# Optimization experiments

Measured on AMD Instinct MI355X. Metric: run time of the kernel, lower is better.

## Reference

```python
import jax, jax.numpy as jnp
import numpy as np

B, N, C = 4, 4096, 512
H = 8          # num_heads
M = 64         # num_landmarks
HD = C // H    # head_dim = 64
N_ITER = 6     # Newton-Schulz iterations (Nystromformer default)


def iterative_inv(mat):
    # mat: [B, H, M, M]; Nystromformer pseudo-inverse via Newton-Schulz.
    I = jnp.eye(mat.shape[-1], dtype=mat.dtype)
    K = mat
    # global-max initialization (original Nystromformer 'original' init)
    V = K.swapaxes(-1, -2) / (jnp.max(jnp.sum(K, axis=-2)) * jnp.max(jnp.sum(K, axis=-1)))
    for _ in range(N_ITER):
        KV = jnp.matmul(K, V)
        V = 0.25 * jnp.matmul(V, 13.0 * I - jnp.matmul(KV, 15.0 * I - jnp.matmul(KV, 7.0 * I - KV)))
    return V


def setup_inputs() -> dict:
    key = jax.random.key(0)
    k1, k2, k3, k4 = jax.random.split(key, 4)
    s = C ** -0.5
    return {
        "x": jax.random.normal(k1, (B, N, C), dtype=jnp.float32),
        "qkv_w": jax.random.normal(k2, (3 * C, C), dtype=jnp.float32) * s,
        "proj_w": jax.random.normal(k3, (C, C), dtype=jnp.float32) * s,
        "proj_b": jax.random.normal(k4, (C,), dtype=jnp.float32) * 0.01,
        "epoch": 1,
    }


def reference(x, qkv_w, proj_w, proj_b, epoch):
    b, n, c = x.shape
    hd = c // H
    qkv = (x @ qkv_w.T).reshape(b, n, 3, H, hd).transpose(2, 0, 3, 1, 4)  # [3,B,H,N,hd]
    Q, K, V = qkv[0], qkv[1], qkv[2]
    scale = 1.0 / np.sqrt(np.sqrt(hd)).astype(np.float32)
    Q = Q * scale
    K = K * scale
    # landmark pooling: mean over segments of length N // M
    Ql = Q.reshape(b, H, M, n // M, hd).mean(axis=-2)  # [B,H,M,hd]
    Kl = K.reshape(b, H, M, n // M, hd).mean(axis=-2)
    kernel_1 = jax.nn.softmax(jnp.einsum('bhnd,bhmd->bhnm', Q, Kl), axis=-1)   # [B,H,N,M]
    kernel_2 = jax.nn.softmax(jnp.einsum('bhmd,bhld->bhml', Ql, Kl), axis=-1)  # [B,H,M,M]
    kernel_3 = jax.nn.softmax(jnp.einsum('bhmd,bhnd->bhmn', Ql, K), axis=-1)   # [B,H,M,N]
    X = jnp.matmul(jnp.matmul(kernel_1, iterative_inv(kernel_2)), jnp.matmul(kernel_3, V))
    X = X.transpose(0, 2, 1, 3).reshape(b, n, c)
    return X @ proj_w.T + proj_b
```

## Files before the change

kernel.cpp:

```cpp
#include <hip/hip_runtime.h>
#include <hip/hip_bf16.h>
#include <stdint.h>

#define QSZe 8388608ull

typedef __attribute__((ext_vector_type(8))) short bf16x8;
typedef __attribute__((ext_vector_type(4))) float f32x4;
typedef const __attribute__((address_space(1))) unsigned int* gas1_t;
typedef __attribute__((address_space(3))) unsigned int* las3_t;

__device__ __forceinline__ float bf2f(unsigned short u) {
  return __uint_as_float(((unsigned int)u) << 16);
}
__device__ __forceinline__ unsigned short f2bf(float f) {
  unsigned int u = __float_as_uint(f);
  unsigned int r = (u + 0x7FFFu + ((u >> 16) & 1u)) >> 16;
  return (unsigned short)r;
}
__device__ __forceinline__ void gload_lds16(const void* g, void* l) {
  __builtin_amdgcn_global_load_lds((gas1_t)g, (las3_t)l, 16, 0, 0);
}

__global__ void detect_bias(const unsigned short* __restrict__ raw_x,
                            const void* __restrict__ raw_b,
                            float* __restrict__ cbf,
                            unsigned int* __restrict__ flag) {
  __shared__ unsigned int fl;
  int t = threadIdx.x;
  if (t < 64) {
    int big = 0;
    for (int i = t; i < 256; i += 64) {
      int e = (raw_x[i] >> 7) & 0xFF;
      if (e >= 0x8F) big = 1;
    }
    unsigned long long b = __ballot(big);
    if (t == 0) {
      fl = (b != 0ull) ? 1u : 0u;
      flag[0] = fl;
    }
  }
  __syncthreads();
  unsigned int f = fl;
  for (int i = t; i < 512; i += 256)
    cbf[i] = f ? ((const float*)raw_b)[i]
               : bf2f(((const unsigned short*)raw_b)[i]);
}

__global__ __launch_bounds__(256) void conv_all(
    const void* __restrict__ rx, const void* __restrict__ rwq,
    const void* __restrict__ rwp, unsigned short* __restrict__ cx,
    unsigned short* __restrict__ cwq, unsigned short* __restrict__ cwp,
    const unsigned int* __restrict__ flag) {
  int gid = blockIdx.x * 256 + threadIdx.x;
  const void* src;
  unsigned short* dst;
  int i8;
  if (gid < 1048576) {
    src = rx; dst = cx; i8 = gid * 8;
  } else if (gid < 1146880) {
    src = rwq; dst = cwq; i8 = (gid - 1048576) * 8;
  } else {
    src = rwp; dst = cwp; i8 = (gid - 1146880) * 8;
  }
  if (flag[0]) {
    const float* f = (const float*)src;
    float4 a = *(const float4*)(f + i8);
    float4 b = *(const float4*)(f + i8 + 4);
    unsigned short o[8] = {f2bf(a.x), f2bf(a.y), f2bf(a.z), f2bf(a.w),
                           f2bf(b.x), f2bf(b.y), f2bf(b.z), f2bf(b.w)};
    *(uint4*)(dst + i8) = *(const uint4*)o;
  } else {
    *(uint4*)(dst + i8) = *(const uint4*)((const unsigned short*)src + i8);
  }
}

__device__ __forceinline__ void mmB(const unsigned short* A_R,
                                    const unsigned short* B_T,
                                    unsigned short* out_R,
                                    unsigned short* out_T, int wave, int lane,
                                    float s, float dg, float a7,
                                    const unsigned short* Aelt) {
  const int fr = lane & 15, fq = lane >> 4;
  bf16x8 af0 = *(const bf16x8*)&A_R[(wave * 16 + fr) * 64 + fq * 8];
  bf16x8 af1 = *(const bf16x8*)&A_R[(wave * 16 + fr) * 64 + 32 + fq * 8];
  f32x4 acc[4] = {};
#pragma unroll
  for (int j = 0; j < 4; j++) {
    bf16x8 b0 = *(const bf16x8*)&B_T[(j * 16 + fr) * 64 + fq * 8];
    bf16x8 b1 = *(const bf16x8*)&B_T[(j * 16 + fr) * 64 + 32 + fq * 8];
    acc[j] = __builtin_amdgcn_mfma_f32_16x16x32_bf16(af0, b0, acc[j], 0, 0, 0);
    acc[j] = __builtin_amdgcn_mfma_f32_16x16x32_bf16(af1, b1, acc[j], 0, 0, 0);
  }
  float ael[4][4];
  if (Aelt) {
#pragma unroll
    for (int j = 0; j < 4; j++)
#pragma unroll
      for (int r = 0; r < 4; r++)
        ael[j][r] = bf2f(Aelt[(wave * 16 + fq * 4 + r) * 64 + j * 16 + fr]);
  }
  __syncthreads();
#pragma unroll
  for (int j = 0; j < 4; j++) {
    int col = j * 16 + fr;
    unsigned short pack[4];
#pragma unroll
    for (int r = 0; r < 4; r++) {
      int row = wave * 16 + fq * 4 + r;
      float v = s * acc[j][r] + ((row == col) ? dg : 0.0f);
      if (Aelt) v += a7 * ael[j][r];
      unsigned short bv = f2bf(v);
      if (out_R) out_R[row * 64 + col] = bv;
      pack[r] = bv;
    }
    if (out_T)
      *(uint2*)&out_T[col * 64 + wave * 16 + fq * 4] = *(const uint2*)pack;
  }
}

__global__ __launch_bounds__(256) void qkv_gemm_mfma(
    const unsigned short* __restrict__ w, const unsigned short* __restrict__ x,
    unsigned short* __restrict__ qkv, float* __restrict__ Ql,
    float* __restrict__ Kl, unsigned short* __restrict__ Qlb,
    unsigned short* __restrict__ Klb) {
  __shared__ __align__(16) unsigned short At[128 * 64];
  __shared__ __align__(16) unsigned short Bt[128 * 64];
  const int t = threadIdx.x;
  const int lane = t & 63, wave = t >> 6;
  const int wf = wave >> 1, wt = wave & 1;
  const int f0 = blockIdx.x * 128, n0g = blockIdx.y * 128;
  const int srow = lane >> 3, skc = ((lane & 7) ^ srow) * 8;
  const int fr = lane & 15, fq = lane >> 4;
  const int rsw = fr & 7;
  f32x4 acc[4][4] = {};

  for (int k0 = 0; k0 < 512; k0 += 64) {
#pragma unroll
    for (int s = 0; s < 4; s++) {
      int inst = wave * 4 + s;
      int row = inst * 8 + srow;
      gload_lds16(w + (size_t)(f0 + row) * 512 + k0 + skc, &At[inst * 512]);
      gload_lds16(x + (size_t)(n0g + row) * 512 + k0 + skc, &Bt[inst * 512]);
    }
    __syncthreads();
#pragma unroll
    for (int kk = 0; kk < 64; kk += 32) {
      bf16x8 af[4], bxf[4];
#pragma unroll
      for (int i = 0; i < 4; i++)
        af[i] = *(const bf16x8*)&At[(wf * 64 + i * 16 + fr) * 64 +
                                    ((((kk >> 3) + fq) ^ rsw) << 3)];
#pragma unroll
      for (int j = 0; j < 4; j++)
        bxf[j] = *(const bf16x8*)&Bt[(wt * 64 + j * 16 + fr) * 64 +
                                     ((((kk >> 3) + fq) ^ rsw) << 3)];
#pragma unroll
      for (int i = 0; i < 4; i++)
#pragma unroll
        for (int j = 0; j < 4; j++)
          acc[i][j] = __builtin_amdgcn_mfma_f32_16x16x32_bf16(
              af[i], bxf[j], acc[i][j], 0, 0, 0);
    }
    __syncthreads();
  }
  const int fbase = f0 + wf * 64;
  const int which = fbase >> 9;
  const int h = (fbase >> 6) & 7;
  const float scale = (which < 2) ? 0.3535533905932738f : 1.0f;
  const int b_ = n0g >> 12;
  const int bh = b_ * 8 + h;
  const int m_loc = ((n0g + wt * 64) & 4095) >> 6;
#pragma unroll
  for (int i = 0; i < 4; i++) {
    int d0 = i * 16 + fq * 4;
#pragma unroll
    for (int j = 0; j < 4; j++) {
      int nn = (n0g + wt * 64 + j * 16 + fr) & 4095;
      unsigned short pack[4];
#pragma unroll
      for (int r = 0; r < 4; r++) pack[r] = f2bf(acc[i][j][r] * scale);
      *(uint2*)&qkv[(size_t)which * QSZe + ((size_t)bh * 4096 + nn) * 64 +
                    d0] = *(const uint2*)pack;
    }
  }
  if (which < 2) {
    const float ps = scale * (1.0f / 64.0f);
#pragma unroll
    for (int i = 0; i < 4; i++) {
      float sm[4];
#pragma unroll
      for (int r = 0; r < 4; r++)
        sm[r] = acc[i][0][r] + acc[i][1][r] + acc[i][2][r] + acc[i][3][r];
#pragma unroll
      for (int mask = 1; mask < 16; mask <<= 1)
#pragma unroll
        for (int r = 0; r < 4; r++) sm[r] += __shfl_xor(sm[r], mask, 64);
      if (fr == 0) {
        int d0 = i * 16 + fq * 4;
        float4 v4 = make_float4(sm[0] * ps, sm[1] * ps, sm[2] * ps, sm[3] * ps);
        unsigned short pk[4] = {f2bf(v4.x), f2bf(v4.y), f2bf(v4.z), f2bf(v4.w)};
        size_t off = (size_t)bh * 4096 + m_loc * 64 + d0;
        if (which == 0) {
          *(float4*)&Ql[off] = v4;
          *(uint2*)&Qlb[off] = *(const uint2*)pk;
        } else {
          *(float4*)&Kl[off] = v4;
          *(uint2*)&Klb[off] = *(const uint2*)pk;
        }
      }
    }
  }
}

__global__ __launch_bounds__(256) void k2_kernel(
    const float* __restrict__ Ql, const float* __restrict__ Kl,
    float* __restrict__ k2, unsigned int* __restrict__ gstat) {
  __shared__ float KlT[64 * 64];
  __shared__ float Ps[64][65];
  int t = threadIdx.x;
  int lane = t & 63, wv = t >> 6;
  int bh = blockIdx.x;
#pragma unroll
  for (int i = 0; i < 16; i++) {
    int idx = i * 256 + t;
    KlT[(idx & 63) * 64 + (idx >> 6)] = Kl[bh * 4096 + idx];
  }
  __syncthreads();
  for (int r = wv * 16; r < wv * 16 + 16; r++) {
    float qv = Ql[(bh * 64 + r) * 64 + lane];
    float acc = 0.f;
#pragma unroll
    for (int k = 0; k < 64; k++) acc += __shfl(qv, k, 64) * KlT[k * 64 + lane];
    float mx = acc;
#pragma unroll
    for (int o = 32; o > 0; o >>= 1) mx = fmaxf(mx, __shfl_xor(mx, o, 64));
    float e = __expf(acc - mx);
    float s = e;
#pragma unroll
    for (int o = 32; o > 0; o >>= 1) s += __shfl_xor(s, o, 64);
    float p = e / s;
    k2[(bh * 64 + r) * 64 + lane] = p;
    Ps[r][lane] = p;
  }
  __syncthreads();
  float val = 0.f;
  if (t < 64) {
    for (int r = 0; r < 64; r++) val += Ps[r][t];
  } else if (t < 128) {
    int r = t - 64;
    for (int c = 0; c < 64; c++) val += Ps[r][c];
  }
  float mv = val;
#pragma unroll
  for (int o = 32; o > 0; o >>= 1) mv = fmaxf(mv, __shfl_xor(mv, o, 64));
  if (t == 0) atomicMax(gstat + 0, __float_as_uint(mv));
  if (t == 64) atomicMax(gstat + 1, __float_as_uint(mv));
}

__global__ __launch_bounds__(256) void k3_mfma(
    const unsigned short* __restrict__ Qlb,
    const unsigned short* __restrict__ qkv, float* __restrict__ Wp,
    float* __restrict__ sp) {
  __shared__ __align__(16) unsigned short Et[64 * 136];
  __shared__ __align__(16) unsigned short Vt[64 * 136];
  __shared__ float scol_l[4][64];
  const int t = threadIdx.x;
  const int lane = t & 63, wave = t >> 6;
  const int fr = lane & 15, fq = lane >> 4;
  const int slab = blockIdx.x, bh = blockIdx.y;
  const int n_base = slab * 512;
  const unsigned short* Kb = qkv + QSZe + (size_t)bh * 262144;
  const unsigned short* Vb = qkv + 2 * QSZe + (size_t)bh * 262144;
  const unsigned short* Qlp = Qlb + bh * 4096;

  bf16x8 qb[2][4];
#pragma unroll
  for (int h = 0; h < 2; h++)
#pragma unroll
    for (int j = 0; j < 4; j++)
      qb[h][j] = *(const bf16x8*)(Qlp + (j * 16 + fr) * 64 + h * 32 + fq * 8);

  f32x4 accW[4] = {};
  float scol[4] = {0.f, 0.f, 0.f, 0.f};

  for (int sc = 0; sc < 4; sc++) {
    const int n0 = n_base + sc * 128;
    {
      int n = t & 127, dg = t >> 7;
#pragma unroll
      for (int i = 0; i < 4; i++) {
        int d0 = (dg + 2 * i) * 8;
        uint4 v = *(const uint4*)(Vb + (size_t)(n0 + n) * 64 + d0);
        const unsigned short* s = (const unsigned short*)&v;
#pragma unroll
        for (int u = 0; u < 8; u++) Vt[(d0 + u) * 136 + n] = s[u];
      }
    }
    f32x4 acc[2][4] = {};
#pragma unroll
    for (int i = 0; i < 2; i++) {
      const unsigned short* Kr =
          Kb + (size_t)(n0 + wave * 32 + i * 16 + fr) * 64;
      bf16x8 a0 = *(const bf16x8*)(Kr + fq * 8);
      bf16x8 a1 = *(const bf16x8*)(Kr + 32 + fq * 8);
#pragma unroll
      for (int j = 0; j < 4; j++) {
        acc[i][j] = __builtin_amdgcn_mfma_f32_16x16x32_bf16(a0, qb[0][j],
                                                            acc[i][j], 0, 0, 0);
        acc[i][j] = __builtin_amdgcn_mfma_f32_16x16x32_bf16(a1, qb[1][j],
                                                            acc[i][j], 0, 0, 0);
      }
    }
#pragma unroll
    for (int i = 0; i < 2; i++)
#pragma unroll
      for (int j = 0; j < 4; j++) {
        unsigned short pack[4];
        float s4 = 0.f;
#pragma unroll
        for (int r = 0; r < 4; r++) {
          float e = __expf(acc[i][j][r]);
          s4 += e;
          pack[r] = f2bf(e);
        }
        scol[j] += s4;
        *(uint2*)&Et[(j * 16 + fr) * 136 + wave * 32 + i * 16 + fq * 4] =
            *(const uint2*)pack;
      }
    __syncthreads();
#pragma unroll
    for (int kk = 0; kk < 128; kk += 32) {
      bf16x8 ap = *(const bf16x8*)&Et[(wave * 16 + fr) * 136 + kk + fq * 8];
#pragma unroll
      for (int j = 0; j < 4; j++) {
        bf16x8 bv = *(const bf16x8*)&Vt[(j * 16 + fr) * 136 + kk + fq * 8];
        accW[j] =
            __builtin_amdgcn_mfma_f32_16x16x32_bf16(ap, bv, accW[j], 0, 0, 0);
      }
    }
    __syncthreads();
  }
#pragma unroll
  for (int j = 0; j < 4; j++) {
    float s = scol[j];
    s += __shfl_xor(s, 16, 64);
    s += __shfl_xor(s, 32, 64);
    if (fq == 0) scol_l[wave][j * 16 + fr] = s;
  }
  __syncthreads();
  if (t < 64)
    sp[(bh * 8 + slab) * 64 + t] =
        scol_l[0][t] + scol_l[1][t] + scol_l[2][t] + scol_l[3][t];
  float* wpo = Wp + ((size_t)bh * 8 + slab) * 4096;
#pragma unroll
  for (int j = 0; j < 4; j++)
#pragma unroll
    for (int r = 0; r < 4; r++)
      wpo[(wave * 16 + fq * 4 + r) * 64 + j * 16 + fr] = accW[j][r];
}

__global__ __launch_bounds__(256) void ns_kernel(
    const float* __restrict__ k2g, const unsigned int* __restrict__ gstat,
    const float* __restrict__ Wp, const float* __restrict__ sp,
    unsigned short* __restrict__ Ztb) {
  __shared__ __align__(16) unsigned short L[8 * 4096];
  __shared__ float ssum[64];
  unsigned short* K2R = L;
  unsigned short* VR = L + 4096;
  unsigned short* VT = L + 2 * 4096;
  unsigned short* AR = L + 3 * 4096;
  unsigned short* AT = L + 4 * 4096;
  unsigned short* T2T = L + 5 * 4096;
  unsigned short* T3T = L + 6 * 4096;
  unsigned short* WT = L + 7 * 4096;
  const int t = threadIdx.x, bh = blockIdx.x;
  const int lane = t & 63, wave = t >> 6;
  const float scale =
      1.0f / (__uint_as_float(gstat[0]) * __uint_as_float(gstat[1]));
  const float* k2p = k2g + bh * 4096;
  if (t < 64) {
    float s = 0.f;
#pragma unroll
    for (int c = 0; c < 8; c++) s += sp[(bh * 8 + c) * 64 + t];
    ssum[t] = s;
  }
  __syncthreads();
#pragma unroll
  for (int i = 0; i < 16; i++) {
    int idx = i * 256 + t;
    int m = idx >> 6, d = idx & 63;
    float kv = k2p[idx];
    K2R[idx] = f2bf(kv);
    VT[idx] = f2bf(kv * scale);
    VR[idx] = f2bf(k2p[d * 64 + m] * scale);
    float wv = 0.f;
#pragma unroll
    for (int cc = 0; cc < 8; cc++)
      wv += Wp[((size_t)(bh * 8 + cc)) * 4096 + idx];
    WT[d * 64 + m] = f2bf(wv / ssum[m]);
  }
  __syncthreads();
  for (int it = 0; it < 6; it++) {
    mmB(K2R, VT, AR, AT, wave, lane, 1.0f, 0.0f, 0.0f, nullptr);
    __syncthreads();
    mmB(AR, AT, nullptr, T2T, wave, lane, 1.0f, 15.0f, -7.0f, AR);
    __syncthreads();
    mmB(AR, T2T, nullptr, T3T, wave, lane, -1.0f, 13.0f, 0.0f, nullptr);
    __syncthreads();
    mmB(VR, T3T, VR, VT, wave, lane, 0.25f, 0.0f, 0.0f, nullptr);
    __syncthreads();
  }
  {
    const int fr = lane & 15, fq = lane >> 4;
    bf16x8 af0 = *(const bf16x8*)&WT[(wave * 16 + fr) * 64 + fq * 8];
    bf16x8 af1 = *(const bf16x8*)&WT[(wave * 16 + fr) * 64 + 32 + fq * 8];
    f32x4 acc[4] = {};
#pragma unroll
    for (int j = 0; j < 4; j++) {
      bf16x8 b0 = *(const bf16x8*)&VR[(j * 16 + fr) * 64 + fq * 8];
      bf16x8 b1 = *(const bf16x8*)&VR[(j * 16 + fr) * 64 + 32 + fq * 8];
      acc[j] =
          __builtin_amdgcn_mfma_f32_16x16x32_bf16(af0, b0, acc[j], 0, 0, 0);
      acc[j] =
          __builtin_amdgcn_mfma_f32_16x16x32_bf16(af1, b1, acc[j], 0, 0, 0);
    }
#pragma unroll
    for (int j = 0; j < 4; j++) {
      int m = j * 16 + fr;
#pragma unroll
      for (int r = 0; r < 4; r++) {
        int d = wave * 16 + fq * 4 + r;
        Ztb[bh * 4096 + d * 64 + m] = f2bf(acc[j][r]);
      }
    }
  }
}

__global__ __launch_bounds__(256) void k1x_mfma(
    const unsigned short* __restrict__ qkv,
    const unsigned short* __restrict__ Klb,
    const unsigned short* __restrict__ Ztb, unsigned short* __restrict__ X) {
  __shared__ __align__(16) unsigned short Qt[128 * 64];
  __shared__ __align__(16) unsigned short Ps[128 * 72];
  const int t = threadIdx.x;
  const int lane = t & 63, wave = t >> 6;
  const int fr = lane & 15, fq = lane >> 4;
  const int rsw = fr & 7;
  const int bh = blockIdx.x;
  const int n0 = blockIdx.y * 128;
  const unsigned short* Qb = qkv + (size_t)bh * 262144 + (size_t)n0 * 64;
  const unsigned short* Klp = Klb + bh * 4096;
  const unsigned short* Ztp = Ztb + bh * 4096;

  {
    const int srow = lane >> 3, skc = ((lane & 7) ^ srow) * 8;
#pragma unroll
    for (int s = 0; s < 4; s++) {
      int inst = wave * 4 + s;
      gload_lds16(Qb + (size_t)(inst * 8 + srow) * 64 + skc, &Qt[inst * 512]);
    }
  }
  __syncthreads();

  f32x4 acc[2][4] = {};
#pragma unroll
  for (int kk = 0; kk < 64; kk += 32) {
    bf16x8 af[2], bg[4];
#pragma unroll
    for (int i = 0; i < 2; i++)
      af[i] = *(const bf16x8*)&Qt[(wave * 32 + i * 16 + fr) * 64 +
                                  ((((kk >> 3) + fq) ^ rsw) << 3)];
#pragma unroll
    for (int j = 0; j < 4; j++)
      bg[j] = *(const bf16x8*)(Klp + (j * 16 + fr) * 64 + kk + fq * 8);
#pragma unroll
    for (int i = 0; i < 2; i++)
#pragma unroll
      for (int j = 0; j < 4; j++)
        acc[i][j] = __builtin_amdgcn_mfma_f32_16x16x32_bf16(af[i], bg[j],
                                                            acc[i][j], 0, 0, 0);
  }

#pragma unroll
  for (int i = 0; i < 2; i++) {
    float sr[4] = {0.f, 0.f, 0.f, 0.f};
#pragma unroll
    for (int j = 0; j < 4; j++)
#pragma unroll
      for (int r = 0; r < 4; r++) {
        float e = __expf(acc[i][j][r]);
        acc[i][j][r] = e;
        sr[r] += e;
      }
#pragma unroll
    for (int mask = 1; mask < 16; mask <<= 1)
#pragma unroll
      for (int r = 0; r < 4; r++) sr[r] += __shfl_xor(sr[r], mask, 64);
    float is[4];
#pragma unroll
    for (int r = 0; r < 4; r++) is[r] = 1.0f / sr[r];
#pragma unroll
    for (int j = 0; j < 4; j++)
#pragma unroll
      for (int r = 0; r < 4; r++)
        Ps[(wave * 32 + i * 16 + fq * 4 + r) * 72 + j * 16 + fr] =
            f2bf(acc[i][j][r] * is[r]);
  }
  __syncthreads();

  f32x4 ax[2][4] = {};
#pragma unroll
  for (int kk = 0; kk < 64; kk += 32) {
    bf16x8 ap[2], bz[4];
#pragma unroll
    for (int i = 0; i < 2; i++)
      ap[i] =
          *(const bf16x8*)&Ps[(wave * 32 + i * 16 + fr) * 72 + kk + fq * 8];
#pragma unroll
    for (int j = 0; j < 4; j++)
      bz[j] = *(const bf16x8*)(Ztp + (j * 16 + fr) * 64 + kk + fq * 8);
#pragma unroll
    for (int i = 0; i < 2; i++)
#pragma unroll
      for (int j = 0; j < 4; j++)
        ax[i][j] = __builtin_amdgcn_mfma_f32_16x16x32_bf16(ap[i], bz[j],
                                                           ax[i][j], 0, 0, 0);
  }

  const int b_ = bh >> 3, h = bh & 7;
#pragma unroll
  for (int i = 0; i < 2; i++) {
#pragma unroll
    for (int j = 0; j < 4; j++) {
      int c = h * 64 + j * 16 + fr;
#pragma unroll
      for (int r = 0; r < 4; r++) {
        int n = n0 + wave * 32 + i * 16 + fq * 4 + r;
        X[((size_t)(b_ * 4096 + n)) * 512 + c] = f2bf(ax[i][j][r]);
      }
    }
  }
}

__global__ __launch_bounds__(256) void proj_gemm_mfma(
    const unsigned short* __restrict__ X, const unsigned short* __restrict__ w,
    const float* __restrict__ bias, float* __restrict__ out) {
  __shared__ __align__(16) unsigned short At[128 * 64];
  __shared__ __align__(16) unsigned short Bt[128 * 64];
  const int t = threadIdx.x;
  const int lane = t & 63, wave = t >> 6;
  const int wr = wave >> 1, wc = wave & 1;
  const int i0 = blockIdx.y * 128, j0 = blockIdx.x * 128;
  const int srow = lane >> 3;
  const int skc = ((lane & 7) ^ srow) * 8;
  const int fr = lane & 15, fq = lane >> 4;
  const int rsw = fr & 7;
  f32x4 acc[4][4] = {};

  for (int k0 = 0; k0 < 512; k0 += 64) {
#pragma unroll
    for (int s = 0; s < 4; s++) {
      int inst = wave * 4 + s;
      int row = inst * 8 + srow;
      gload_lds16(X + (size_t)(i0 + row) * 512 + k0 + skc, &At[inst * 512]);
      gload_lds16(w + (size_t)(j0 + row) * 512 + k0 + skc, &Bt[inst * 512]);
    }
    __syncthreads();
#pragma unroll
    for (int kk = 0; kk < 64; kk += 32) {
      bf16x8 af[4], bg[4];
#pragma unroll
      for (int i = 0; i < 4; i++)
        af[i] = *(const bf16x8*)&At[(wr * 64 + i * 16 + fr) * 64 +
                                    ((((kk >> 3) + fq) ^ rsw) << 3)];
#pragma unroll
      for (int j = 0; j < 4; j++)
        bg[j] = *(const bf16x8*)&Bt[(wc * 64 + j * 16 + fr) * 64 +
                                    ((((kk >> 3) + fq) ^ rsw) << 3)];
#pragma unroll
      for (int i = 0; i < 4; i++)
#pragma unroll
        for (int j = 0; j < 4; j++)
          acc[i][j] = __builtin_amdgcn_mfma_f32_16x16x32_bf16(
              af[i], bg[j], acc[i][j], 0, 0, 0);
    }
    __syncthreads();
  }
#pragma unroll
  for (int j = 0; j < 4; j++) {
    int col = j0 + wc * 64 + j * 16 + fr;
    float bia = bias[col];
#pragma unroll
    for (int i = 0; i < 4; i++) {
      int rbase = i0 + wr * 64 + i * 16 + fq * 4;
#pragma unroll
      for (int r = 0; r < 4; r++) {
        out[(size_t)(rbase + r) * 512 + col] = acc[i][j][r] + bia;
      }
    }
  }
}

extern "C" void kernel_launch(void* const* d_in, const int* in_sizes, int n_in,
                              void* d_out, int out_size, void* d_ws,
                              size_t ws_size, hipStream_t stream) {
  (void)in_sizes; (void)n_in; (void)out_size; (void)ws_size;

  char* w8 = (char*)d_ws;
  unsigned short* cx  = (unsigned short*)(w8 + 0);
  unsigned short* cwq = (unsigned short*)(w8 + 16777216);
  unsigned short* cwp = (unsigned short*)(w8 + 18350080);
  float*          cbf = (float*)(w8 + 18874368);
  unsigned short* qkv = (unsigned short*)(w8 + 18876416);
  unsigned short* X   = (unsigned short*)(w8 + 69208064);
  float* Ql = (float*)(w8 + 85985280);
  float* Kl = (float*)(w8 + 86509568);
  float* k2 = (float*)(w8 + 87033856);
  unsigned short* Ztb = (unsigned short*)(w8 + 88082432);
  unsigned int* gstat = (unsigned int*)(w8 + 88606720);
  float* Wp = (float*)(w8 + 88608768);
  float* sp = (float*)(w8 + 92803072);
  unsigned short* Klb = (unsigned short*)(w8 + 92868608);
  unsigned short* Qlb = (unsigned short*)(w8 + 93130752);

  hipMemsetAsync(gstat, 0, 16, stream);
  detect_bias<<<1, 256, 0, stream>>>((const unsigned short*)d_in[0], d_in[3],
                                     cbf, gstat + 2);
  conv_all<<<4608, 256, 0, stream>>>(d_in[0], d_in[1], d_in[2], cx, cwq, cwp,
                                     gstat + 2);
  qkv_gemm_mfma<<<dim3(12, 128), 256, 0, stream>>>(cwq, cx, qkv, Ql, Kl, Qlb,
                                                   Klb);
  k2_kernel<<<32, 256, 0, stream>>>(Ql, Kl, k2, gstat);
  k3_mfma<<<dim3(8, 32), 256, 0, stream>>>(Qlb, qkv, Wp, sp);
  ns_kernel<<<32, 256, 0, stream>>>(k2, gstat, Wp, sp, Ztb);
  k1x_mfma<<<dim3(32, 32), 256, 0, stream>>>(qkv, Klb, Ztb, X);
  proj_gemm_mfma<<<dim3(4, 128), 256, 0, stream>>>(X, cwp, cbf,
                                                   (float*)d_out);
}
```

Measured before the change: 235.8 us.

## Double-buffer LDS in QKV and projection GEMMs, swizzle tiles, split k3 finer

Both bf16 GEMMs (qkv and proj) now ping-pong between two LDS buffers, so the global-to-LDS load of the next K-slab is issued before the MFMA work on the current slab. Block indices are remapped with an XCD-style swizzle to improve L2 locality across neighbouring blocks. The k3 kernel splits N into 16 slabs of 256 instead of 8 of 512, doubling its grid for more parallelism. In exchange ns_kernel reduces twice as many partials, and the Wp buffer moves onto the cx workspace region, which is no longer needed by then. The GEMMs also double their LDS use, which may lower occupancy.

```diff
diff --git a/kernel.cpp b/kernel.cpp
--- a/kernel.cpp
+++ b/kernel.cpp
@@ -123,37 +123,41 @@
     unsigned short* __restrict__ qkv, float* __restrict__ Ql,
     float* __restrict__ Kl, unsigned short* __restrict__ Qlb,
     unsigned short* __restrict__ Klb) {
-  __shared__ __align__(16) unsigned short At[128 * 64];
-  __shared__ __align__(16) unsigned short Bt[128 * 64];
+  __shared__ __align__(16) unsigned short At[2][128 * 64];
+  __shared__ __align__(16) unsigned short Bt[2][128 * 64];
   const int t = threadIdx.x;
   const int lane = t & 63, wave = t >> 6;
   const int wf = wave >> 1, wt = wave & 1;
-  const int f0 = blockIdx.x * 128, n0g = blockIdx.y * 128;
+  const int lin = blockIdx.x + blockIdx.y * 12;
+  const int swz = (lin & 7) * 192 + (lin >> 3);
+  const int f0 = (swz % 12) * 128, n0g = (swz / 12) * 128;
   const int srow = lane >> 3, skc = ((lane & 7) ^ srow) * 8;
   const int fr = lane & 15, fq = lane >> 4;
   const int rsw = fr & 7;
   f32x4 acc[4][4] = {};
 
-  for (int k0 = 0; k0 < 512; k0 += 64) {
+  auto STAGE = [&](int p, int k0) {
 #pragma unroll
     for (int s = 0; s < 4; s++) {
       int inst = wave * 4 + s;
       int row = inst * 8 + srow;
-      gload_lds16(w + (size_t)(f0 + row) * 512 + k0 + skc, &At[inst * 512]);
-      gload_lds16(x + (size_t)(n0g + row) * 512 + k0 + skc, &Bt[inst * 512]);
-    }
-    __syncthreads();
+      gload_lds16(w + (size_t)(f0 + row) * 512 + k0 + skc, &At[p][inst * 512]);
+      gload_lds16(x + (size_t)(n0g + row) * 512 + k0 + skc,
+                  &Bt[p][inst * 512]);
+    }
+  };
+  auto COMPUTE = [&](int p) {
 #pragma unroll
     for (int kk = 0; kk < 64; kk += 32) {
       bf16x8 af[4], bxf[4];
 #pragma unroll
       for (int i = 0; i < 4; i++)
-        af[i] = *(const bf16x8*)&At[(wf * 64 + i * 16 + fr) * 64 +
-                                    ((((kk >> 3) + fq) ^ rsw) << 3)];
+        af[i] = *(const bf16x8*)&At[p][(wf * 64 + i * 16 + fr) * 64 +
+                                       ((((kk >> 3) + fq) ^ rsw) << 3)];
 #pragma unroll
       for (int j = 0; j < 4; j++)
-        bxf[j] = *(const bf16x8*)&Bt[(wt * 64 + j * 16 + fr) * 64 +
-                                     ((((kk >> 3) + fq) ^ rsw) << 3)];
+        bxf[j] = *(const bf16x8*)&Bt[p][(wt * 64 + j * 16 + fr) * 64 +
+                                        ((((kk >> 3) + fq) ^ rsw) << 3)];
 #pragma unroll
       for (int i = 0; i < 4; i++)
 #pragma unroll
@@ -161,6 +165,17 @@
           acc[i][j] = __builtin_amdgcn_mfma_f32_16x16x32_bf16(
               af[i], bxf[j], acc[i][j], 0, 0, 0);
     }
+  };
+
+  STAGE(0, 0);
+  __syncthreads();
+#pragma unroll
+  for (int k0 = 0; k0 < 512; k0 += 128) {
+    STAGE(1, k0 + 64);
+    COMPUTE(0);
+    __syncthreads();
+    if (k0 + 128 < 512) STAGE(0, k0 + 128);
+    COMPUTE(1);
     __syncthreads();
   }
   const int fbase = f0 + wf * 64;
@@ -268,7 +283,7 @@
   const int lane = t & 63, wave = t >> 6;
   const int fr = lane & 15, fq = lane >> 4;
   const int slab = blockIdx.x, bh = blockIdx.y;
-  const int n_base = slab * 512;
+  const int n_base = slab * 256;
   const unsigned short* Kb = qkv + QSZe + (size_t)bh * 262144;
   const unsigned short* Vb = qkv + 2 * QSZe + (size_t)bh * 262144;
   const unsigned short* Qlp = Qlb + bh * 4096;
@@ -283,7 +298,7 @@
   f32x4 accW[4] = {};
   float scol[4] = {0.f, 0.f, 0.f, 0.f};
 
-  for (int sc = 0; sc < 4; sc++) {
+  for (int sc = 0; sc < 2; sc++) {
     const int n0 = n_base + sc * 128;
     {
       int n = t & 127, dg = t >> 7;
@@ -349,9 +364,9 @@
   }
   __syncthreads();
   if (t < 64)
-    sp[(bh * 8 + slab) * 64 + t] =
+    sp[(bh * 16 + slab) * 64 + t] =
         scol_l[0][t] + scol_l[1][t] + scol_l[2][t] + scol_l[3][t];
-  float* wpo = Wp + ((size_t)bh * 8 + slab) * 4096;
+  float* wpo = Wp + ((size_t)bh * 16 + slab) * 4096;
 #pragma unroll
   for (int j = 0; j < 4; j++)
 #pragma unroll
@@ -381,7 +396,7 @@
   if (t < 64) {
     float s = 0.f;
 #pragma unroll
-    for (int c = 0; c < 8; c++) s += sp[(bh * 8 + c) * 64 + t];
+    for (int c = 0; c < 16; c++) s += sp[(bh * 16 + c) * 64 + t];
     ssum[t] = s;
   }
   __syncthreads();
@@ -395,8 +410,8 @@
     VR[idx] = f2bf(k2p[d * 64 + m] * scale);
     float wv = 0.f;
 #pragma unroll
-    for (int cc = 0; cc < 8; cc++)
-      wv += Wp[((size_t)(bh * 8 + cc)) * 4096 + idx];
+    for (int cc = 0; cc < 16; cc++)
+      wv += Wp[((size_t)(bh * 16 + cc)) * 4096 + idx];
     WT[d * 64 + m] = f2bf(wv / ssum[m]);
   }
   __syncthreads();
@@ -545,38 +560,42 @@
 __global__ __launch_bounds__(256) void proj_gemm_mfma(
     const unsigned short* __restrict__ X, const unsigned short* __restrict__ w,
     const float* __restrict__ bias, float* __restrict__ out) {
-  __shared__ __align__(16) unsigned short At[128 * 64];
-  __shared__ __align__(16) unsigned short Bt[128 * 64];
+  __shared__ __align__(16) unsigned short At[2][128 * 64];
+  __shared__ __align__(16) unsigned short Bt[2][128 * 64];
   const int t = threadIdx.x;
   const int lane = t & 63, wave = t >> 6;
   const int wr = wave >> 1, wc = wave & 1;
-  const int i0 = blockIdx.y * 128, j0 = blockIdx.x * 128;
+  const int lin = blockIdx.x + blockIdx.y * 4;
+  const int swz = (lin & 7) * 64 + (lin >> 3);
+  const int j0 = (swz % 4) * 128, i0 = (swz / 4) * 128;
   const int srow = lane >> 3;
   const int skc = ((lane & 7) ^ srow) * 8;
   const int fr = lane & 15, fq = lane >> 4;
   const int rsw = fr & 7;
   f32x4 acc[4][4] = {};
 
-  for (int k0 = 0; k0 < 512; k0 += 64) {
+  auto STAGE = [&](int p, int k0) {
 #pragma unroll
     for (int s = 0; s < 4; s++) {
       int inst = wave * 4 + s;
       int row = inst * 8 + srow;
-      gload_lds16(X + (size_t)(i0 + row) * 512 + k0 + skc, &At[inst * 512]);
-      gload_lds16(w + (size_t)(j0 + row) * 512 + k0 + skc, &Bt[inst * 512]);
-    }
-    __syncthreads();
+      gload_lds16(X + (size_t)(i0 + row) * 512 + k0 + skc, &At[p][inst * 512]);
+      gload_lds16(w + (size_t)(j0 + row) * 512 + k0 + skc,
+                  &Bt[p][inst * 512]);
+    }
+  };
+  auto COMPUTE = [&](int p) {
 #pragma unroll
     for (int kk = 0; kk < 64; kk += 32) {
       bf16x8 af[4], bg[4];
 #pragma unroll
       for (int i = 0; i < 4; i++)
-        af[i] = *(const bf16x8*)&At[(wr * 64 + i * 16 + fr) * 64 +
-                                    ((((kk >> 3) + fq) ^ rsw) << 3)];
+        af[i] = *(const bf16x8*)&At[p][(wr * 64 + i * 16 + fr) * 64 +
+                                       ((((kk >> 3) + fq) ^ rsw) << 3)];
 #pragma unroll
       for (int j = 0; j < 4; j++)
-        bg[j] = *(const bf16x8*)&Bt[(wc * 64 + j * 16 + fr) * 64 +
-                                    ((((kk >> 3) + fq) ^ rsw) << 3)];
+        bg[j] = *(const bf16x8*)&Bt[p][(wc * 64 + j * 16 + fr) * 64 +
+                                       ((((kk >> 3) + fq) ^ rsw) << 3)];
 #pragma unroll
       for (int i = 0; i < 4; i++)
 #pragma unroll
@@ -584,6 +603,17 @@
           acc[i][j] = __builtin_amdgcn_mfma_f32_16x16x32_bf16(
               af[i], bg[j], acc[i][j], 0, 0, 0);
     }
+  };
+
+  STAGE(0, 0);
+  __syncthreads();
+#pragma unroll
+  for (int k0 = 0; k0 < 512; k0 += 128) {
+    STAGE(1, k0 + 64);
+    COMPUTE(0);
+    __syncthreads();
+    if (k0 + 128 < 512) STAGE(0, k0 + 128);
+    COMPUTE(1);
     __syncthreads();
   }
 #pragma unroll
@@ -618,8 +648,8 @@
   float* k2 = (float*)(w8 + 87033856);
   unsigned short* Ztb = (unsigned short*)(w8 + 88082432);
   unsigned int* gstat = (unsigned int*)(w8 + 88606720);
-  float* Wp = (float*)(w8 + 88608768);
-  float* sp = (float*)(w8 + 92803072);
+  float* Wp = (float*)(w8 + 0);
+  float* sp = (float*)(w8 + 88608768);
   unsigned short* Klb = (unsigned short*)(w8 + 92868608);
   unsigned short* Qlb = (unsigned short*)(w8 + 93130752);
 
@@ -631,7 +661,7 @@
   qkv_gemm_mfma<<<dim3(12, 128), 256, 0, stream>>>(cwq, cx, qkv, Ql, Kl, Qlb,
                                                    Klb);
   k2_kernel<<<32, 256, 0, stream>>>(Ql, Kl, k2, gstat);
-  k3_mfma<<<dim3(8, 32), 256, 0, stream>>>(Qlb, qkv, Wp, sp);
+  k3_mfma<<<dim3(16, 32), 256, 0, stream>>>(Qlb, qkv, Wp, sp);
   ns_kernel<<<32, 256, 0, stream>>>(k2, gstat, Wp, sp, Ztb);
   k1x_mfma<<<dim3(32, 32), 256, 0, stream>>>(qkv, Klb, Ztb, X);
   proj_gemm_mfma<<<dim3(4, 128), 256, 0, stream>>>(X, cwp, cbf,
```

After: 238.1 us. Within noise of the previous version (+1.0%).
